# Kernel optimization log

Hardware: AMD Instinct MI355X
Metric: run time of the kernel (lower is better)

## Reference

```python
import jax, jax.numpy as jnp
import numpy as np

# QTIP QuantizedLinear config (decode_mode='lut')
IN_F, OUT_F = 4096, 4096
TD_X, TD_Y = 16, 16          # weight tile
L, K, V = 16, 2, 2           # trellis state bits, bits/weight, values/state
TLUT_BITS = 16               # lut mode: tlut_bits == L


def fwht(x):
    """Normalized fast Walsh-Hadamard transform over the last axis (power of 2).
    Equivalent to matmul_hadU with K=1 (features are powers of two)."""
    n = x.shape[-1]
    h = 1
    while h < n:
        x = x.reshape(x.shape[:-1] + (n // (2 * h), 2, h))
        a, b = x[..., 0, :], x[..., 1, :]
        x = jnp.stack([a + b, a - b], axis=-2).reshape(x.shape[:-3] + (n,))
        h *= 2
    return x / jnp.sqrt(jnp.float32(n))


def dequantize_weight(trellis, tlut):
    """Bitshift trellis decode: each 16x16 tile stores td_x*td_y*K = 512 bits.
    The stream is walked KV = K*V bits per step (tail-biting); each L-bit state
    indexes the LUT producing V weights. trellis holds uint16 words in int32."""
    num_tiles = trellis.shape[0]
    T = TD_X * TD_Y            # 256 weights per tile
    S = T // V                 # 128 trellis steps per tile
    KV = K * V                 # 4 fresh bits per step
    steps = L // KV            # 4 nibbles form one L-bit state
    words = trellis & 0xFFFF
    bit_pos = jnp.arange(15, -1, -1)                     # MSB-first within word
    bits = (words[:, :, None] >> bit_pos) & 1            # (tiles, 32, 16)
    nib_w = 2 ** jnp.arange(KV - 1, -1, -1)
    nibs = jnp.sum(bits.reshape(num_tiles, S, KV) * nib_w, axis=-1)  # (tiles, S)
    # state_i = (nib[i-3]<<12)|(nib[i-2]<<8)|(nib[i-1]<<4)|nib[i], wraparound (tail-biting)
    states = jnp.zeros_like(nibs)
    for j in range(steps):
        states = states | (jnp.roll(nibs, j, axis=1) << (KV * j))
    vals = tlut[states]                                  # (tiles, S, V)
    W = vals.reshape(OUT_F // TD_X, IN_F // TD_Y, TD_X, TD_Y)
    return W.transpose(0, 2, 1, 3).reshape(OUT_F, IN_F)


def setup_inputs() -> dict:
    key = jax.random.key(0)
    k1, k2, k3, k4, k5 = jax.random.split(key, 5)
    inp = jax.random.normal(k1, (8, 2048, IN_F), jnp.float32)
    num_tiles = (OUT_F // TD_X) * (IN_F // TD_Y)
    words = (TD_X * TD_Y * K + 15) // 16
    trellis = jax.random.randint(k2, (num_tiles, words), 0, 65536, jnp.int32)
    tlut = jax.random.normal(k3, (2 ** TLUT_BITS, V), jnp.float32)
    SU = jax.random.normal(k4, (IN_F,), jnp.float32)
    SV = jax.random.normal(k5, (OUT_F,), jnp.float32)
    return {"input": inp, "trellis": trellis, "tlut": tlut, "SU": SU, "SV": SV}


def reference(input, trellis, tlut, SU, SV):
    W = dequantize_weight(trellis, tlut)          # (OUT_F, IN_F)
    x = input.reshape(-1, IN_F) * SU              # input rescale (sign vector)
    x = fwht(x)                                   # left Hadamard rotation
    x = x @ W.T                                   # fused dequant matmul
    x = fwht(x)                                   # right Hadamard rotation
    x = x * SV                                    # output rescale
    return x.reshape(input.shape[:-1] + (OUT_F,))
```

## Files before the change

kernel.cpp:

```cpp
#include <hip/hip_runtime.h>

typedef __attribute__((ext_vector_type(8))) short short8;
typedef __attribute__((ext_vector_type(4))) float f32x4;

__device__ __forceinline__ unsigned short f2bf(float f) {
  union { float f; unsigned u; } x{f};
  unsigned r = x.u + 0x7FFFu + ((x.u >> 16) & 1u);
  return (unsigned short)(r >> 16);
}

__device__ __forceinline__ void gload_lds16(const void* g, void* l) {
  __builtin_amdgcn_global_load_lds(
      (__attribute__((address_space(1))) void*)((unsigned long long)g),
      (__attribute__((address_space(3))) void*)(unsigned)((unsigned long long)l),
      16, 0, 0);
}

__device__ __forceinline__ void butterfly64(float (*tile)[64], int t) {
  const int c  = t & 63;
  const int pb = t >> 6;
#pragma unroll
  for (int h = 1; h < 64; h <<= 1) {
#pragma unroll
    for (int k = 0; k < 8; ++k) {
      const int p  = pb + (k << 2);
      const int j1 = ((p & ~(h - 1)) << 1) | (p & (h - 1));
      const int j2 = j1 + h;
      const float a = tile[j1][c], b = tile[j2][c];
      tile[j1][c] = a + b;
      tile[j2][c] = a - b;
    }
    __syncthreads();
  }
}

__global__ void k_deq_col1(const int* __restrict__ trellis,
                           const float* __restrict__ tlut,
                           float* __restrict__ W) {
  __shared__ unsigned short words[16][32];
  __shared__ float tile[64][64];
  const int t  = threadIdx.x;
  const int rg = blockIdx.x >> 6;
  const int cg = blockIdx.x & 63;
#pragma unroll
  for (int r = 0; r < 2; ++r) {
    const int ff = t + (r << 8);
    const int a = ff >> 7, rw = ff & 127;
    const int src = ((rg * 4 + a) * 256 + cg * 4) * 32 + rw;
    ((unsigned short*)words)[a * 128 + rw] = (unsigned short)(trellis[src] & 0xFFFF);
  }
  __syncthreads();
#pragma unroll
  for (int r = 0; r < 8; ++r) {
    const int f  = t + (r << 8);
    const int tl = f >> 7, s = f & 127;
    const unsigned short* w = words[tl];
    unsigned state = 0;
#pragma unroll
    for (int j = 0; j < 4; ++j) {
      const int ss = (s - j) & 127;
      state |= (((unsigned)w[ss >> 2] >> (12 - 4 * (ss & 3))) & 0xFu) << (4 * j);
    }
    const float2 v = *(const float2*)(tlut + (size_t)state * 2);
    const int o = ((tl >> 2) << 4) + (s >> 3);
    const int i = ((tl & 3) << 4) + ((s & 7) << 1);
    tile[o][i]     = v.x;
    tile[o][i + 1] = v.y;
  }
  __syncthreads();
  butterfly64(tile, t);
  const size_t base = ((size_t)(rg * 64)) * 4096 + cg * 64;
#pragma unroll
  for (int k = 0; k < 4; ++k) {
    const int idx = t + (k << 8);
    const int r = idx >> 4, c4 = idx & 15;
    *(float4*)(W + base + (size_t)r * 4096 + (c4 << 2)) = *(float4*)(&tile[r][c4 << 2]);
  }
}

__global__ void k_fwht_row(float* __restrict__ W) {
  __shared__ float row[4096];
  const int t = threadIdx.x;
  float* g = W + ((size_t)blockIdx.x << 12);
#pragma unroll
  for (int k = 0; k < 4; ++k) {
    const int e = (t + (k << 8)) << 2;
    *(float4*)(row + e) = *(const float4*)(g + e);
  }
  __syncthreads();
  for (int h = 1; h < 4096; h <<= 1) {
#pragma unroll
    for (int k = 0; k < 8; ++k) {
      const int p  = t + (k << 8);
      const int j1 = ((p & ~(h - 1)) << 1) | (p & (h - 1));
      const int j2 = j1 + h;
      const float a = row[j1], b = row[j2];
      row[j1] = a + b;
      row[j2] = a - b;
    }
    __syncthreads();
  }
#pragma unroll
  for (int k = 0; k < 4; ++k) {
    const int e = (t + (k << 8)) << 2;
    float4 v = *(float4*)(row + e);
    v.x *= 0.015625f; v.y *= 0.015625f; v.z *= 0.015625f; v.w *= 0.015625f;
    *(float4*)(g + e) = v;
  }
}

__global__ void k_fwht_col2(const float* __restrict__ W,
                            const float* __restrict__ SU,
                            const float* __restrict__ SV,
                            unsigned short* __restrict__ Mt) {
  __shared__ float tile[64][64];
  const int t  = threadIdx.x;
  const int b  = blockIdx.x >> 6;
  const int cg = blockIdx.x & 63;
#pragma unroll
  for (int k = 0; k < 4; ++k) {
    const int idx = t + (k << 8);
    const int a = idx >> 4, c4 = idx & 15;
    const int row = (a << 6) + b;
    *(float4*)(&tile[a][c4 << 2]) =
        *(const float4*)(W + (size_t)row * 4096 + ((size_t)cg << 6) + (c4 << 2));
  }
  __syncthreads();
  butterfly64(tile, t);
#pragma unroll
  for (int k = 0; k < 4; ++k) {
    const int idx = t + (k << 8);
    const int a = idx >> 4, c4 = idx & 15;
    const int row = (a << 6) + b;
    const int col0 = (cg << 6) + (c4 << 2);
    const float sv = SV[row] * 0.015625f;
    const float4 su = *(const float4*)(SU + col0);
    const float4 v = *(float4*)(&tile[a][c4 << 2]);
    ushort4 o;
    o.x = f2bf(v.x * sv * su.x);
    o.y = f2bf(v.y * sv * su.y);
    o.z = f2bf(v.z * sv * su.z);
    o.w = f2bf(v.w * sv * su.w);
    *(ushort4*)(Mt + (size_t)row * 4096 + col0) = o;
  }
}

__global__ void k_cvt_x(const float* __restrict__ x, unsigned short* __restrict__ xb) {
  const long long n4 = (long long)16384 * 4096 / 4;
  long long i = (long long)blockIdx.x * blockDim.x + threadIdx.x;
  const long long stride = (long long)gridDim.x * blockDim.x;
  for (; i < n4; i += stride) {
    const float4 v = *(const float4*)(x + i * 4);
    ushort4 o;
    o.x = f2bf(v.x); o.y = f2bf(v.y); o.z = f2bf(v.z); o.w = f2bf(v.w);
    *(ushort4*)(xb + i * 4) = o;
  }
}

#define BARRIER __builtin_amdgcn_s_barrier()
#define WAITV0  asm volatile("s_waitcnt vmcnt(0)" ::: "memory")

#define STAGE_ALL(db, jj) do { \
  const unsigned short* aJ = aRow + ((jj) << 6); \
  const unsigned short* bJ = bRow + ((jj) << 6); \
  gload_lds16(aJ,                  smem +         (db)*32768 +         w1k); \
  gload_lds16(aJ + ( 64ull << 12), smem +         (db)*32768 +  8192 + w1k); \
  gload_lds16(aJ + (128ull << 12), smem +         (db)*32768 + 16384 + w1k); \
  gload_lds16(aJ + (192ull << 12), smem +         (db)*32768 + 24576 + w1k); \
  gload_lds16(bJ,                  smem + 65536 + (db)*32768 +         w1k); \
  gload_lds16(bJ + ( 64ull << 12), smem + 65536 + (db)*32768 +  8192 + w1k); \
  gload_lds16(bJ + (128ull << 12), smem + 65536 + (db)*32768 + 16384 + w1k); \
  gload_lds16(bJ + (192ull << 12), smem + 65536 + (db)*32768 + 24576 + w1k); \
} while (0)

#define HALF_K(Asx, Bsx, cx) do { \
  bb[0] = *(const short8*)((Bsx) + 0*2048 + (cx)); \
  bb[1] = *(const short8*)((Bsx) + 1*2048 + (cx)); \
  bb[2] = *(const short8*)((Bsx) + 2*2048 + (cx)); \
  bb[3] = *(const short8*)((Bsx) + 3*2048 + (cx)); \
  short8 acur = *(const short8*)((Asx) + 0*2048 + (cx)); \
  _Pragma("unroll") \
  for (int mi = 0; mi < 8; ++mi) { \
    short8 anxt = acur; \
    if (mi < 7) anxt = *(const short8*)((Asx) + (mi + 1) * 2048 + (cx)); \
    acc[mi][0] = __builtin_amdgcn_mfma_f32_16x16x32_bf16(acur, bb[0], acc[mi][0], 0, 0, 0); \
    acc[mi][1] = __builtin_amdgcn_mfma_f32_16x16x32_bf16(acur, bb[1], acc[mi][1], 0, 0, 0); \
    acc[mi][2] = __builtin_amdgcn_mfma_f32_16x16x32_bf16(acur, bb[2], acc[mi][2], 0, 0, 0); \
    acc[mi][3] = __builtin_amdgcn_mfma_f32_16x16x32_bf16(acur, bb[3], acc[mi][3], 0, 0, 0); \
    acur = anxt; \
  } \
} while (0)

#define KTILE(Asx, Bsx, STAGES) do { \
  WAITV0; BARRIER; \
  STAGES; \
  HALF_K(Asx, Bsx, cx0); \
  HALF_K(Asx, Bsx, cx1); \
} while (0)

__global__ void __launch_bounds__(512, 2)
k_gemm8(const unsigned short* __restrict__ A,
        const unsigned short* __restrict__ B,
        float* __restrict__ C) {
  extern __shared__ char smem[];
  const int t    = threadIdx.x;
  const int lane = t & 63, w = t >> 6;
  const int wr   = w >> 2, wc = w & 3;
  const int hb   = wc >> 1, rb = (wc & 1) * 64;
  const int lr   = lane & 15, q = lane >> 4;
  const int w1k  = w * 1024;

  const int bid = ((blockIdx.x & 7) << 7) + (blockIdx.x >> 3);
  const int nt  = bid & 15;
  const int mt  = bid >> 4;

  const int cx0 = lr * 128 + (((0 + q) ^ (lr & 7)) << 4);
  const int cx1 = lr * 128 + (((4 + q) ^ (lr & 7)) << 4);

  const char* As0 = smem +         wr * 16384;
  const char* As1 = smem + 32768 + wr * 16384;
  const char* Bs0 = smem + 65536 +         hb * 16384 + rb * 128;
  const char* Bs1 = smem + 65536 + 32768 + hb * 16384 + rb * 128;

  const int srow  = t >> 3;
  const int csrc8 = (((t & 7) ^ (srow & 7)) << 3);
  const unsigned short* aRow = A + (((size_t)(mt * 256 + srow)) << 12) + csrc8;
  const unsigned short* bRow = B + (((size_t)(nt * 256 + srow)) << 12) + csrc8;

  short8 bb[4];
  f32x4  acc[8][4];
#pragma unroll
  for (int i = 0; i < 8; ++i)
#pragma unroll
    for (int j = 0; j < 4; ++j) acc[i][j] = (f32x4){0.f, 0.f, 0.f, 0.f};

  STAGE_ALL(0, 0);

  for (int g = 0; g < 31; ++g) {
    KTILE(As0, Bs0, STAGE_ALL(1, 2 * g + 1));
    KTILE(As1, Bs1, STAGE_ALL(0, 2 * g + 2));
  }
  KTILE(As0, Bs0, STAGE_ALL(1, 63));
  KTILE(As1, Bs1, {});

  float* cbase = C + (((size_t)(mt * 256 + wr * 128 + q * 4)) << 12)
               + nt * 256 + wc * 64 + lr;
#pragma unroll
  for (int mi = 0; mi < 8; ++mi)
#pragma unroll
    for (int ni = 0; ni < 4; ++ni)
#pragma unroll
      for (int r = 0; r < 4; ++r)
        cbase[(((size_t)(mi * 16 + r)) << 12) + ni * 16] = acc[mi][ni][r];
}

extern "C" void kernel_launch(void* const* d_in, const int* in_sizes, int n_in,
                              void* d_out, int out_size, void* d_ws, size_t ws_size,
                              hipStream_t stream) {
  const float* x       = (const float*)d_in[0];
  const int*   trellis = (const int*)d_in[1];
  const float* tlut    = (const float*)d_in[2];
  const float* SU      = (const float*)d_in[3];
  const float* SV      = (const float*)d_in[4];
  float* out = (float*)d_out;

  char* ws = (char*)d_ws;
  float*          W  = (float*)ws;
  unsigned short* Mt = (unsigned short*)(ws + (64ull << 20));
  unsigned short* xb = (unsigned short*)(ws + (96ull << 20));

  hipFuncSetAttribute(reinterpret_cast<const void*>(&k_gemm8),
                      hipFuncAttributeMaxDynamicSharedMemorySize, 131072);

  hipLaunchKernelGGL(k_deq_col1,  dim3(4096),  dim3(256), 0, stream, trellis, tlut, W);
  hipLaunchKernelGGL(k_fwht_row,  dim3(4096),  dim3(256), 0, stream, W);
  hipLaunchKernelGGL(k_fwht_col2, dim3(4096),  dim3(256), 0, stream, W, SU, SV, Mt);
  hipLaunchKernelGGL(k_cvt_x,     dim3(2048),  dim3(256), 0, stream, x, xb);
  hipLaunchKernelGGL(k_gemm8,     dim3(1024),  dim3(512), 131072, stream, xb, Mt, out);
}
```

Measured before the change: 691.5 us.

## Switch GEMM to 4-stage K=32 LDS pipeline with partial vmcnt waits

The bf16 GEMM main loop changes from a double-buffered K=64 tile to a 4-deep ring of K=32 tiles. Each step waits only for the oldest stage with a partial vmcnt instead of draining all loads, which lets global-to-LDS loads overlap with compute. It also preloads all A and B fragments before the MFMA block, wraps the MFMAs in s_setprio, changes the LDS swizzle, and drops the block-index remapping used for L2 locality. The cost is twice as many barriers per K and more fragment registers, with the new swizzle and the lost raster order as possible regressions.

```diff
diff --git a/kernel.cpp b/kernel.cpp
--- a/kernel.cpp
+++ b/kernel.cpp
@@ -158,44 +158,38 @@
 }
 
 #define BARRIER __builtin_amdgcn_s_barrier()
-#define WAITV0  asm volatile("s_waitcnt vmcnt(0)" ::: "memory")
-
-#define STAGE_ALL(db, jj) do { \
-  const unsigned short* aJ = aRow + ((jj) << 6); \
-  const unsigned short* bJ = bRow + ((jj) << 6); \
-  gload_lds16(aJ,                  smem +         (db)*32768 +         w1k); \
-  gload_lds16(aJ + ( 64ull << 12), smem +         (db)*32768 +  8192 + w1k); \
-  gload_lds16(aJ + (128ull << 12), smem +         (db)*32768 + 16384 + w1k); \
-  gload_lds16(aJ + (192ull << 12), smem +         (db)*32768 + 24576 + w1k); \
-  gload_lds16(bJ,                  smem + 65536 + (db)*32768 +         w1k); \
-  gload_lds16(bJ + ( 64ull << 12), smem + 65536 + (db)*32768 +  8192 + w1k); \
-  gload_lds16(bJ + (128ull << 12), smem + 65536 + (db)*32768 + 16384 + w1k); \
-  gload_lds16(bJ + (192ull << 12), smem + 65536 + (db)*32768 + 24576 + w1k); \
+
+#define STAGE(buf, jj) do { \
+  const unsigned short* aJ = aRow + ((jj) << 5); \
+  const unsigned short* bJ = bRow + ((jj) << 5); \
+  gload_lds16(aJ,                  smem +         (buf)*16384 +        w1k); \
+  gload_lds16(aJ + (128ull << 12), smem +         (buf)*16384 + 8192 + w1k); \
+  gload_lds16(bJ,                  smem + 65536 + (buf)*16384 +        w1k); \
+  gload_lds16(bJ + (128ull << 12), smem + 65536 + (buf)*16384 + 8192 + w1k); \
 } while (0)
 
-#define HALF_K(Asx, Bsx, cx) do { \
-  bb[0] = *(const short8*)((Bsx) + 0*2048 + (cx)); \
-  bb[1] = *(const short8*)((Bsx) + 1*2048 + (cx)); \
-  bb[2] = *(const short8*)((Bsx) + 2*2048 + (cx)); \
-  bb[3] = *(const short8*)((Bsx) + 3*2048 + (cx)); \
-  short8 acur = *(const short8*)((Asx) + 0*2048 + (cx)); \
+#define RD_AB(buf) do { _Pragma("unroll") \
+  for (int ni = 0; ni < 4; ++ni) \
+    bb[ni] = *(const short8*)(smem + 65536 + (buf)*16384 + wc4k + ni*1024 + cx); \
   _Pragma("unroll") \
+  for (int mi = 0; mi < 8; ++mi) \
+    af[mi] = *(const short8*)(smem +         (buf)*16384 + wr8k + mi*1024 + cx); \
+} while (0)
+
+#define MMA32 do { _Pragma("unroll") \
   for (int mi = 0; mi < 8; ++mi) { \
-    short8 anxt = acur; \
-    if (mi < 7) anxt = *(const short8*)((Asx) + (mi + 1) * 2048 + (cx)); \
-    acc[mi][0] = __builtin_amdgcn_mfma_f32_16x16x32_bf16(acur, bb[0], acc[mi][0], 0, 0, 0); \
-    acc[mi][1] = __builtin_amdgcn_mfma_f32_16x16x32_bf16(acur, bb[1], acc[mi][1], 0, 0, 0); \
-    acc[mi][2] = __builtin_amdgcn_mfma_f32_16x16x32_bf16(acur, bb[2], acc[mi][2], 0, 0, 0); \
-    acc[mi][3] = __builtin_amdgcn_mfma_f32_16x16x32_bf16(acur, bb[3], acc[mi][3], 0, 0, 0); \
-    acur = anxt; \
-  } \
-} while (0)
-
-#define KTILE(Asx, Bsx, STAGES) do { \
-  WAITV0; BARRIER; \
+    acc[mi][0] = __builtin_amdgcn_mfma_f32_16x16x32_bf16(af[mi], bb[0], acc[mi][0], 0, 0, 0); \
+    acc[mi][1] = __builtin_amdgcn_mfma_f32_16x16x32_bf16(af[mi], bb[1], acc[mi][1], 0, 0, 0); \
+    acc[mi][2] = __builtin_amdgcn_mfma_f32_16x16x32_bf16(af[mi], bb[2], acc[mi][2], 0, 0, 0); \
+    acc[mi][3] = __builtin_amdgcn_mfma_f32_16x16x32_bf16(af[mi], bb[3], acc[mi][3], 0, 0, 0); \
+  } } while (0)
+
+#define KT(buf, STAGES, WN) do { \
+  asm volatile("s_waitcnt vmcnt(" #WN ")" ::: "memory"); \
+  BARRIER; \
   STAGES; \
-  HALF_K(Asx, Bsx, cx0); \
-  HALF_K(Asx, Bsx, cx1); \
+  RD_AB(buf); \
+  __builtin_amdgcn_s_setprio(1); MMA32; __builtin_amdgcn_s_setprio(0); \
 } while (0)
 
 __global__ void __launch_bounds__(512, 2)
@@ -206,42 +200,40 @@
   const int t    = threadIdx.x;
   const int lane = t & 63, w = t >> 6;
   const int wr   = w >> 2, wc = w & 3;
-  const int hb   = wc >> 1, rb = (wc & 1) * 64;
   const int lr   = lane & 15, q = lane >> 4;
   const int w1k  = w * 1024;
-
-  const int bid = ((blockIdx.x & 7) << 7) + (blockIdx.x >> 3);
-  const int nt  = bid & 15;
-  const int mt  = bid >> 4;
-
-  const int cx0 = lr * 128 + (((0 + q) ^ (lr & 7)) << 4);
-  const int cx1 = lr * 128 + (((4 + q) ^ (lr & 7)) << 4);
-
-  const char* As0 = smem +         wr * 16384;
-  const char* As1 = smem + 32768 + wr * 16384;
-  const char* Bs0 = smem + 65536 +         hb * 16384 + rb * 128;
-  const char* Bs1 = smem + 65536 + 32768 + hb * 16384 + rb * 128;
-
-  const int srow  = t >> 3;
-  const int csrc8 = (((t & 7) ^ (srow & 7)) << 3);
+  const int wr8k = wr * 8192, wc4k = wc * 4096;
+
+  const int nt = blockIdx.x & 15;
+  const int mt = blockIdx.x >> 4;
+
+  const int cx = lr * 64 + ((q ^ ((lr >> 1) & 3)) << 4);
+
+  const int srow  = t >> 2;
+  const int csrc8 = (((t & 3) ^ ((t >> 3) & 3)) << 3);
   const unsigned short* aRow = A + (((size_t)(mt * 256 + srow)) << 12) + csrc8;
   const unsigned short* bRow = B + (((size_t)(nt * 256 + srow)) << 12) + csrc8;
 
-  short8 bb[4];
+  short8 af[8], bb[4];
   f32x4  acc[8][4];
 #pragma unroll
   for (int i = 0; i < 8; ++i)
 #pragma unroll
     for (int j = 0; j < 4; ++j) acc[i][j] = (f32x4){0.f, 0.f, 0.f, 0.f};
 
-  STAGE_ALL(0, 0);
+  STAGE(0, 0); STAGE(1, 1); STAGE(2, 2);
 
   for (int g = 0; g < 31; ++g) {
-    KTILE(As0, Bs0, STAGE_ALL(1, 2 * g + 1));
-    KTILE(As1, Bs1, STAGE_ALL(0, 2 * g + 2));
-  }
-  KTILE(As0, Bs0, STAGE_ALL(1, 63));
-  KTILE(As1, Bs1, {});
+    const int j = 4 * g;
+    KT(0, STAGE(3, j + 3), 8);
+    KT(1, STAGE(0, j + 4), 8);
+    KT(2, STAGE(1, j + 5), 8);
+    KT(3, STAGE(2, j + 6), 8);
+  }
+  KT(0, STAGE(3, 127), 8);
+  KT(1, {},            8);
+  KT(2, {},            4);
+  KT(3, {},            0);
 
   float* cbase = C + (((size_t)(mt * 256 + wr * 128 + q * 4)) << 12)
                + nt * 256 + wc * 64 + lr;
```

After: 648.4 us. -6.2%, faster.
